# Kernel tuning notes

Hardware: AMD Instinct MI355X
Metric: run time of the kernel (lower is better)

## Reference

```python
import jax, jax.numpy as jnp
from jax import lax
import numpy as np

D_MODEL = 1024
D_STATE = 16
D_CONV = 4
EXPAND = 2
D_INNER = EXPAND * D_MODEL          # 2048
DT_RANK = D_MODEL // 16             # 64 (mamba 'auto' dt_rank)
B, L = 1, 1024


def setup_inputs() -> dict:
    key = jax.random.key(0)
    ks = jax.random.split(key, 8)

    def nrm(k, shape, s=0.02):
        return jax.random.normal(k, shape, jnp.float32) * s

    def mamba_params(kbase):
        k = jax.random.split(kbase, 7)
        return {
            'in_w': nrm(k[0], (2 * D_INNER, D_MODEL)),            # in_proj (no bias)
            'conv_w': nrm(k[1], (D_INNER, 1, D_CONV), 0.1),       # depthwise causal conv
            'conv_b': nrm(k[2], (D_INNER,), 0.1),
            'xproj_w': nrm(k[3], (DT_RANK + 2 * D_STATE, D_INNER)),
            'dt_w': nrm(k[4], (D_INNER, DT_RANK), 0.1),
            'dt_b': nrm(k[5], (D_INNER,), 0.1),
            'Alog': jnp.log(jnp.broadcast_to(jnp.arange(1., D_STATE + 1, dtype=jnp.float32), (D_INNER, D_STATE))),
            'Dp': jnp.ones((D_INNER,), jnp.float32),
            'out_w': nrm(k[6], (D_MODEL, D_INNER)),
        }

    fw = mamba_params(ks[0])
    bw = mamba_params(ks[1])
    inp = {'x': jax.random.normal(ks[2], (B, L, D_MODEL), jnp.float32)}
    for n, p in fw.items():
        inp['fw_' + n] = p
    for n, p in bw.items():
        inp['bw_' + n] = p
    inp['proj_w'] = nrm(ks[3], (D_MODEL, 2 * D_MODEL))
    inp['proj_b'] = jnp.zeros((D_MODEL,), jnp.float32)
    inp['ln_w'] = jnp.ones((D_MODEL,), jnp.float32)
    inp['ln_b'] = jnp.zeros((D_MODEL,), jnp.float32)
    return inp


def _mamba(x, in_w, conv_w, conv_b, xproj_w, dt_w, dt_b, Alog, Dp, out_w):
    # x: [B, L, d_model]
    xz = x @ in_w.T                                    # [B, L, 2*d_inner]
    xi, z = jnp.split(xz, 2, axis=-1)
    # causal depthwise conv over time
    xc = lax.conv_general_dilated(jnp.swapaxes(xi, 1, 2), conv_w, (1,),
                                  [(D_CONV - 1, 0)], feature_group_count=D_INNER)
    u = jnp.swapaxes(jax.nn.silu(xc + conv_b[None, :, None]), 1, 2)   # [B, L, d_inner]
    x_dbl = u @ xproj_w.T                              # [B, L, dt_rank + 2*d_state]
    dt = x_dbl[..., :DT_RANK]
    Bm = x_dbl[..., DT_RANK:DT_RANK + D_STATE]
    Cm = x_dbl[..., DT_RANK + D_STATE:]
    delta = jax.nn.softplus(dt @ dt_w.T + dt_b)        # [B, L, d_inner]
    A = -jnp.exp(Alog)                                 # [d_inner, d_state]
    dA = jnp.exp(jnp.einsum('bld,dn->bldn', delta, A))
    dBu = jnp.einsum('bld,bln,bld->bldn', delta, Bm, u)

    def step(h, inputs):
        a, b, c = inputs                               # a,b: [B,D,N]; c: [B,N]
        h = a * h + b
        return h, jnp.einsum('bdn,bn->bd', h, c)

    h0 = jnp.zeros((x.shape[0], D_INNER, D_STATE), x.dtype)
    _, ys = lax.scan(step, h0, (jnp.moveaxis(dA, 1, 0), jnp.moveaxis(dBu, 1, 0), jnp.moveaxis(Cm, 1, 0)))
    y = jnp.moveaxis(ys, 0, 1) + u * Dp                # [B, L, d_inner]
    return (y * jax.nn.silu(z)) @ out_w.T              # [B, L, d_model]


def _block(x,
           fw_in_w, fw_conv_w, fw_conv_b, fw_xproj_w, fw_dt_w, fw_dt_b, fw_Alog, fw_Dp, fw_out_w,
           bw_in_w, bw_conv_w, bw_conv_b, bw_xproj_w, bw_dt_w, bw_dt_b, bw_Alog, bw_Dp, bw_out_w,
           proj_w, proj_b, ln_w, ln_b):
    out_fw = _mamba(x, fw_in_w, fw_conv_w, fw_conv_b, fw_xproj_w, fw_dt_w, fw_dt_b, fw_Alog, fw_Dp, fw_out_w) + x
    xb = jnp.flip(x, axis=1)
    out_bw = jnp.flip(_mamba(xb, bw_in_w, bw_conv_w, bw_conv_b, bw_xproj_w, bw_dt_w, bw_dt_b, bw_Alog, bw_Dp, bw_out_w) + xb, axis=1)
    out = jnp.concatenate([out_fw, out_bw], axis=-1) @ proj_w.T + proj_b
    mu = out.mean(-1, keepdims=True)
    var = out.var(-1, keepdims=True)
    return (out - mu) / jnp.sqrt(var + 1e-5) * ln_w + ln_b


def reference(x,
              fw_in_w, fw_conv_w, fw_conv_b, fw_xproj_w, fw_dt_w, fw_dt_b, fw_Alog, fw_Dp, fw_out_w,
              bw_in_w, bw_conv_w, bw_conv_b, bw_xproj_w, bw_dt_w, bw_dt_b, bw_Alog, bw_Dp, bw_out_w,
              proj_w, proj_b, ln_w, ln_b):
    return _block(x,
                  fw_in_w, fw_conv_w, fw_conv_b, fw_xproj_w, fw_dt_w, fw_dt_b, fw_Alog, fw_Dp, fw_out_w,
                  bw_in_w, bw_conv_w, bw_conv_b, bw_xproj_w, bw_dt_w, bw_dt_b, bw_Alog, bw_Dp, bw_out_w,
                  proj_w, proj_b, ln_w, ln_b)
```

## Files before the change

kernel.cpp:

```cpp
#include <hip/hip_runtime.h>

typedef __bf16 bf16;
typedef __bf16 bf16x8 __attribute__((ext_vector_type(8)));
typedef float  f32x4  __attribute__((ext_vector_type(4)));

#define L_SEQ 1024
#define DM    1024
#define DI    2048
#define DTR   64
#define DSTATE 16
#define XD    96
#define NC    64
#define CS    16

__device__ __forceinline__ float bf2f(bf16 v){ return (float)v; }
__device__ __forceinline__ bf16  f2bf(float v){ return (bf16)v; }

__device__ __forceinline__ void gl_lds16(const bf16* g, bf16* l) {
  __builtin_amdgcn_global_load_lds(
      (const __attribute__((address_space(1))) unsigned int*)g,
      (__attribute__((address_space(3))) unsigned int*)l, 16, 0, 0);
}

#define OFF_X      0L
#define OFF_INW    1048576L
#define OFF_XPROJ  9437184L
#define OFF_DTW    9830400L
#define OFF_OUTW   10092544L
#define OFF_PROJW  14286848L
#define CVT_TOTAL  16384000L

__global__ __launch_bounds__(256) void cvt_k(
    const float* __restrict__ x,
    const float* __restrict__ inw0, const float* __restrict__ inw1,
    const float* __restrict__ xp0,  const float* __restrict__ xp1,
    const float* __restrict__ dt0,  const float* __restrict__ dt1,
    const float* __restrict__ ow0,  const float* __restrict__ ow1,
    const float* __restrict__ pw,   bf16* __restrict__ wb)
{
  long i = ((long)blockIdx.x * 256 + threadIdx.x) * 8;
  if (i >= CVT_TOTAL) return;
  const float* src; long off;
  if      (i < OFF_INW)                 { src = x;    off = i - OFF_X; }
  else if (i < OFF_INW + 4194304L)      { src = inw0; off = i - OFF_INW; }
  else if (i < OFF_XPROJ)               { src = inw1; off = i - (OFF_INW + 4194304L); }
  else if (i < OFF_XPROJ + 196608L)     { src = xp0;  off = i - OFF_XPROJ; }
  else if (i < OFF_DTW)                 { src = xp1;  off = i - (OFF_XPROJ + 196608L); }
  else if (i < OFF_DTW + 131072L)       { src = dt0;  off = i - OFF_DTW; }
  else if (i < OFF_OUTW)                { src = dt1;  off = i - (OFF_DTW + 131072L); }
  else if (i < OFF_OUTW + 2097152L)     { src = ow0;  off = i - OFF_OUTW; }
  else if (i < OFF_PROJW)               { src = ow1;  off = i - (OFF_OUTW + 2097152L); }
  else                                  { src = pw;   off = i - OFF_PROJW; }
  f32x4 v0 = *(const f32x4*)(src + off);
  f32x4 v1 = *(const f32x4*)(src + off + 4);
  bf16x8 t;
  #pragma unroll
  for (int q = 0; q < 4; q++) { t[q] = (bf16)v0[q]; t[4+q] = (bf16)v1[q]; }
  *(bf16x8*)(wb + i) = t;
}

template<int BM, int BN>
__global__ __launch_bounds__(256) void gemm_bt(
    const bf16* __restrict__ A, const bf16* __restrict__ B0, const bf16* __restrict__ B1,
    void* __restrict__ Cv, void* __restrict__ Cv2, int splitN,
    int M, int N, int K, int lda, int ldb, int ldc,
    long aOffZ, long cOffZ,
    const float* __restrict__ bias0, const float* __restrict__ bias1,
    int flipA1, int writeBf16, int act,
    const float* __restrict__ xF, int fuseRes)
{
  constexpr int WM = BM / 2, WN = BN / 2;
  constexpr int MI = WM / 16, NJ = WN / 16;
  constexpr int ACALLS = BM / 32;
  constexpr int BCALLS = BN / 32;

  const int tid  = threadIdx.x;
  const int z    = blockIdx.z;
  const bf16*  Bp   = z ? B1 : B0;
  const float* bias = z ? bias1 : bias0;
  const int flip = z ? flipA1 : 0;
  const int bm = blockIdx.x * BM;
  const int bn = blockIdx.y * BN;

  __shared__ bf16 As[BM * 64];
  __shared__ bf16 Bs[BN * 64];

  f32x4 acc[MI][NJ];
  #pragma unroll
  for (int i=0;i<MI;i++)
    #pragma unroll
    for (int j=0;j<NJ;j++) { acc[i][j][0]=0.f; acc[i][j][1]=0.f; acc[i][j][2]=0.f; acc[i][j][3]=0.f; }

  const int wave = tid >> 6;
  const int lane = tid & 63;
  const int wm = (wave >> 1) * WM;
  const int wn = (wave & 1) * WN;
  const int fr  = lane & 15;
  const int frx = fr & 7;
  const int kqc = lane >> 4;

  const bf16* aSrc[ACALLS];
  int aOff[ACALLS];
  #pragma unroll
  for (int t = 0; t < ACALLS; t++) {
    int s = (wave * ACALLS + t) * 64 + lane;
    int r = s >> 3;
    int j = (s & 7) ^ (r & 7);
    int ar = bm + r;
    int agr = flip ? (M - 1 - ar) : ar;
    aSrc[t] = A + (long)z * aOffZ + (long)agr * lda + j * 8;
    aOff[t] = (wave * ACALLS + t) * 512;
  }
  const bf16* bSrc[BCALLS];
  int bOff[BCALLS];
  #pragma unroll
  for (int t = 0; t < BCALLS; t++) {
    int s = (wave * BCALLS + t) * 64 + lane;
    int r = s >> 3;
    int j = (s & 7) ^ (r & 7);
    int br = bn + r; if (br > N - 1) br = N - 1;
    bSrc[t] = Bp + (long)br * ldb + j * 8;
    bOff[t] = (wave * BCALLS + t) * 512;
  }

  for (int k0 = 0; k0 < K; k0 += 64) {
    #pragma unroll
    for (int t = 0; t < ACALLS; t++) gl_lds16(aSrc[t] + k0, &As[aOff[t]]);
    #pragma unroll
    for (int t = 0; t < BCALLS; t++) gl_lds16(bSrc[t] + k0, &Bs[bOff[t]]);
    __syncthreads();

    #pragma unroll
    for (int ks8 = 0; ks8 < 8; ks8 += 4) {
      bf16x8 af[MI], bfr[NJ];
      #pragma unroll
      for (int i=0;i<MI;i++) {
        int row = wm + i*16 + fr;
        af[i]  = *(const bf16x8*)&As[(row * 8 + ((ks8 + kqc) ^ frx)) * 8];
      }
      #pragma unroll
      for (int j=0;j<NJ;j++) {
        int row = wn + j*16 + fr;
        bfr[j] = *(const bf16x8*)&Bs[(row * 8 + ((ks8 + kqc) ^ frx)) * 8];
      }
      #pragma unroll
      for (int i=0;i<MI;i++)
        #pragma unroll
        for (int j=0;j<NJ;j++)
          acc[i][j] = __builtin_amdgcn_mfma_f32_16x16x32_bf16(af[i], bfr[j], acc[i][j], 0, 0, 0);
    }
    __syncthreads();
  }

  const int rr = (lane >> 4) * 4;
  const int cc = lane & 15;
  #pragma unroll
  for (int i=0;i<MI;i++) {
    #pragma unroll
    for (int j=0;j<NJ;j++) {
      int gn = bn + wn + j*16 + cc;
      if (gn >= N) continue;
      float bv = bias ? bias[gn] : 0.f;
      #pragma unroll
      for (int r=0;r<4;r++) {
        int gm = bm + wm + i*16 + rr + r;
        float v = acc[i][j][r] + bv;
        if (fuseRes) {
          long row = z ? (long)(M - 1 - gm) : (long)gm;
          float o = v + xF[row * DM + gn];
          ((bf16*)Cv)[row * (2 * DM) + (long)z * DM + gn] = f2bf(o);
        } else {
          if (act == 1) v = fmaxf(v, 0.f) + __logf(1.f + __expf(-fabsf(v)));
          int gn2 = gn;
          void* Cp = Cv;
          if (gn >= splitN) { gn2 = gn - splitN; Cp = Cv2; }
          long idx = (long)z * cOffZ + (long)gm * ldc + gn2;
          if (writeBf16) ((bf16*)Cp)[idx] = f2bf(v);
          else           ((float*)Cp)[idx] = v;
        }
      }
    }
  }
}

__global__ __launch_bounds__(256) void conv_silu_k(
    const bf16* __restrict__ xi, const float* __restrict__ cw0, const float* __restrict__ cw1,
    const float* __restrict__ cb0, const float* __restrict__ cb1, bf16* __restrict__ u)
{
  int gid = blockIdx.x * 256 + threadIdx.x;
  int dir = gid >> 18;
  int rem = gid & ((1 << 18) - 1);
  int l = rem >> 8;
  int d0 = (rem & 255) * 8;
  const float* w = dir ? cw1 : cw0;
  const float* b = dir ? cb1 : cb0;
  const bf16* xid = xi + (long)dir * L_SEQ * DI;
  float acc[8];
  #pragma unroll
  for (int q = 0; q < 8; q++) acc[q] = b[d0 + q];
  #pragma unroll
  for (int j = 0; j < 4; j++) {
    int ll = l - 3 + j;
    if (ll < 0) continue;
    bf16x8 xv = *(const bf16x8*)(xid + (long)ll * DI + d0);
    #pragma unroll
    for (int q = 0; q < 8; q++) acc[q] += w[(d0 + q) * 4 + j] * bf2f(xv[q]);
  }
  bf16x8 o;
  #pragma unroll
  for (int q = 0; q < 8; q++) {
    float s = acc[q] / (1.f + __expf(-acc[q]));
    o[q] = f2bf(s);
  }
  *(bf16x8*)(u + (long)dir * L_SEQ * DI + (long)l * DI + d0) = o;
}

__global__ __launch_bounds__(256) void scan_p1(
    const bf16* __restrict__ delta, const bf16* __restrict__ u, const bf16* __restrict__ xdbl,
    const float* __restrict__ Alog0, const float* __restrict__ Alog1,
    bf16* __restrict__ hout, float* __restrict__ sumd)
{
  const int tid = threadIdx.x;
  const int c   = blockIdx.y;
  const int dir = blockIdx.z;
  const int d   = blockIdx.x * 256 + tid;
  const float* Alog = dir ? Alog1 : Alog0;
  const bf16* dl = delta + (long)dir * L_SEQ * DI;
  const bf16* ud = u     + (long)dir * L_SEQ * DI;
  const bf16* xd = xdbl  + (long)dir * L_SEQ * XD;
  const int l0 = c * CS;

  __shared__ float lb[CS][16];
  {
    int ll = tid >> 4, n = tid & 15;
    lb[ll][n] = bf2f(xd[(long)(l0 + ll) * XD + DTR + n]);
  }

  float dl_r[CS], uu_r[CS];
  #pragma unroll
  for (int s = 0; s < CS; s++) {
    dl_r[s] = bf2f(dl[(long)(l0 + s) * DI + d]);
    uu_r[s] = bf2f(ud[(long)(l0 + s) * DI + d]);
  }
  __syncthreads();

  float An[16], h[16];
  #pragma unroll
  for (int n = 0; n < 16; n++) { An[n] = -__expf(Alog[d * 16 + n]); h[n] = 0.f; }
  float sd = 0.f;

  #pragma unroll
  for (int ll = 0; ll < CS; ll++) {
    float dlt = dl_r[ll];
    sd += dlt;
    float du = dlt * uu_r[ll];
    #pragma unroll
    for (int n = 0; n < 16; n++) {
      float a = __expf(dlt * An[n]);
      h[n] = h[n] * a + du * lb[ll][n];
    }
  }

  bf16* hp = hout + (((long)dir * NC + c) * DI + d) * 16;
  bf16x8 o0, o1;
  #pragma unroll
  for (int n = 0; n < 8; n++) { o0[n] = f2bf(h[n]); o1[n] = f2bf(h[8 + n]); }
  *(bf16x8*)hp = o0;
  *(bf16x8*)(hp + 8) = o1;
  sumd[((long)dir * NC + c) * DI + d] = sd;
}

__global__ __launch_bounds__(256) void scan_p2(
    const float* __restrict__ Alog0, const float* __restrict__ Alog1,
    bf16* hout, const float* __restrict__ sumd)
{
  int g = blockIdx.x * 256 + threadIdx.x;
  int dir = g >> 15;
  int rem = g & 32767;
  int d = rem >> 4;
  int n = rem & 15;
  const float* Alog = dir ? Alog1 : Alog0;
  float An = -__expf(Alog[d * 16 + n]);
  float hs = 0.f;
  #pragma unroll 4
  for (int c = 0; c < NC; c++) {
    long base = ((long)dir * NC + c) * DI + d;
    float tmp = bf2f(hout[base * 16 + n]);
    float P = __expf(An * sumd[base]);
    hout[base * 16 + n] = f2bf(hs);
    hs = P * hs + tmp;
  }
}

__global__ __launch_bounds__(256) void scan_p3(
    const bf16* delta, const bf16* zb, const bf16* u, const bf16* __restrict__ xdbl,
    const float* __restrict__ Alog0, const float* __restrict__ Alog1,
    const float* __restrict__ Dp0, const float* __restrict__ Dp1,
    const bf16* __restrict__ hout, bf16* g)
{
  const int tid = threadIdx.x;
  const int c   = blockIdx.y;
  const int dir = blockIdx.z;
  const int d   = blockIdx.x * 256 + tid;
  const float* Alog = dir ? Alog1 : Alog0;
  const float* Dp   = dir ? Dp1 : Dp0;
  const bf16* dl = delta + (long)dir * L_SEQ * DI;
  const bf16* zd = zb    + (long)dir * L_SEQ * DI;
  const bf16* ud = u     + (long)dir * L_SEQ * DI;
  const bf16* xd = xdbl  + (long)dir * L_SEQ * XD;
  bf16* gd = g + (long)dir * L_SEQ * DI;
  const int l0 = c * CS;

  __shared__ float lb[CS][16];
  __shared__ float lc[CS][16];
  {
    int i = tid * 2;
    int ll = i >> 5, j = i & 31;
    const bf16* p = xd + (long)(l0 + ll) * XD + DTR + j;
    float v0 = bf2f(p[0]), v1 = bf2f(p[1]);
    if (j < 16) { lb[ll][j] = v0; lb[ll][j + 1] = v1; }
    else        { lc[ll][j - 16] = v0; lc[ll][j - 15] = v1; }
  }

  float dl_r[CS], uu_r[CS], zv_r[CS];
  #pragma unroll
  for (int s = 0; s < CS; s++) {
    dl_r[s] = bf2f(dl[(long)(l0 + s) * DI + d]);
    zv_r[s] = bf2f(zd[(long)(l0 + s) * DI + d]);
    uu_r[s] = bf2f(ud[(long)(l0 + s) * DI + d]);
  }
  const bf16* hp = hout + (((long)dir * NC + c) * DI + d) * 16;
  bf16x8 h0 = *(const bf16x8*)hp;
  bf16x8 h1 = *(const bf16x8*)(hp + 8);
  __syncthreads();

  float An[16], h[16];
  #pragma unroll
  for (int n = 0; n < 16; n++) {
    An[n] = -__expf(Alog[d * 16 + n]);
    h[n] = bf2f(n < 8 ? h0[n & 7] : h1[n & 7]);
  }
  const float Dpv = Dp[d];

  #pragma unroll
  for (int ll = 0; ll < CS; ll++) {
    float dlt = dl_r[ll];
    float du = dlt * uu_r[ll];
    float y = 0.f;
    #pragma unroll
    for (int n = 0; n < 16; n++) {
      float a = __expf(dlt * An[n]);
      h[n] = h[n] * a + du * lb[ll][n];
      y += h[n] * lc[ll][n];
    }
    y += uu_r[ll] * Dpv;
    float zv = zv_r[ll];
    float sz = zv / (1.f + __expf(-zv));
    gd[(long)(l0 + ll) * DI + d] = f2bf(y * sz);
  }
}

__global__ __launch_bounds__(256) void ln_k(
    const float* __restrict__ fin, const float* __restrict__ pb,
    const float* __restrict__ lnw, const float* __restrict__ lnb, float* __restrict__ out)
{
  int row = blockIdx.x;
  int tid = threadIdx.x;
  float v[4]; float s1 = 0.f, s2 = 0.f;
  #pragma unroll
  for (int j = 0; j < 4; j++) {
    int c = tid + j * 256;
    v[j] = fin[(long)row * DM + c] + pb[c];
    s1 += v[j]; s2 += v[j] * v[j];
  }
  #pragma unroll
  for (int off = 32; off; off >>= 1) { s1 += __shfl_down(s1, off); s2 += __shfl_down(s2, off); }
  __shared__ float red[8];
  int wave = tid >> 6, lane = tid & 63;
  if (lane == 0) { red[wave] = s1; red[4 + wave] = s2; }
  __syncthreads();
  float t1 = red[0] + red[1] + red[2] + red[3];
  float t2 = red[4] + red[5] + red[6] + red[7];
  float mu = t1 / DM;
  float var = t2 / DM - mu * mu;
  float inv = rsqrtf(var + 1e-5f);
  #pragma unroll
  for (int j = 0; j < 4; j++) {
    int c = tid + j * 256;
    out[(long)row * DM + c] = (v[j] - mu) * inv * lnw[c] + lnb[c];
  }
}

extern "C" void kernel_launch(void* const* d_in, const int* in_sizes, int n_in,
                              void* d_out, int out_size, void* d_ws, size_t ws_size,
                              hipStream_t stream)
{
  const float* x         = (const float*)d_in[0];
  const float* fw_conv_w = (const float*)d_in[2];
  const float* fw_conv_b = (const float*)d_in[3];
  const float* fw_dt_b   = (const float*)d_in[6];
  const float* fw_Alog   = (const float*)d_in[7];
  const float* fw_Dp     = (const float*)d_in[8];
  const float* bw_conv_w = (const float*)d_in[11];
  const float* bw_conv_b = (const float*)d_in[12];
  const float* bw_dt_b   = (const float*)d_in[15];
  const float* bw_Alog   = (const float*)d_in[16];
  const float* bw_Dp     = (const float*)d_in[17];
  const float* proj_b    = (const float*)d_in[20];
  const float* ln_w      = (const float*)d_in[21];
  const float* ln_b      = (const float*)d_in[22];

  char* ws = (char*)d_ws;
  const size_t MB = 1024 * 1024;
  bf16*  xi    = (bf16*)(ws + 0);
  bf16*  zb    = (bf16*)(ws + 8 * MB);
  bf16*  u     = (bf16*)(ws + 16 * MB);
  bf16*  xdbl  = (bf16*)(ws + 24 * MB);
  float* sumd  = (float*)(ws + 25 * MB);
  bf16*  hout  = (bf16*)(ws + 26 * MB);
  bf16*  wb    = (bf16*)(ws + 34 * MB);
  bf16*  g     = u;
  bf16*  delta = xi;
  bf16*  fused = (bf16*)(ws + 0);
  float* fin   = (float*)(ws + 4 * MB);

  bf16* xb     = wb + OFF_X;
  bf16* inw    = wb + OFF_INW;
  bf16* xprojw = wb + OFF_XPROJ;
  bf16* dtw    = wb + OFF_DTW;
  bf16* outw   = wb + OFF_OUTW;
  bf16* projw  = wb + OFF_PROJW;

  dim3 blk(256);
  const int BIGN = 1 << 30;

  cvt_k<<<(CVT_TOTAL / 8 + 255) / 256, blk, 0, stream>>>(
      x, (const float*)d_in[1], (const float*)d_in[10],
      (const float*)d_in[4], (const float*)d_in[13],
      (const float*)d_in[5], (const float*)d_in[14],
      (const float*)d_in[9], (const float*)d_in[18],
      (const float*)d_in[19], wb);

  gemm_bt<64,64><<<dim3(16, 64, 2), blk, 0, stream>>>(
      xb, inw, inw + 4194304L, (void*)xi, (void*)zb, 2048,
      1024, 4096, 1024, 1024, 1024, 2048,
      0L, (long)1024 * 2048, nullptr, nullptr, 1, 1, 0, nullptr, 0);

  conv_silu_k<<<2048, blk, 0, stream>>>(xi, fw_conv_w, bw_conv_w, fw_conv_b, bw_conv_b, u);

  gemm_bt<32,64><<<dim3(32, 2, 2), blk, 0, stream>>>(
      u, xprojw, xprojw + 196608L, (void*)xdbl, nullptr, BIGN,
      1024, 96, 2048, 2048, 2048, 96,
      (long)1024 * 2048, (long)1024 * 96, nullptr, nullptr, 0, 1, 0, nullptr, 0);

  gemm_bt<32,64><<<dim3(32, 32, 2), blk, 0, stream>>>(
      xdbl, dtw, dtw + 131072L, (void*)delta, nullptr, BIGN,
      1024, 2048, 64, 96, 64, 2048,
      (long)1024 * 96, (long)1024 * 2048, fw_dt_b, bw_dt_b, 0, 1, 1, nullptr, 0);

  scan_p1<<<dim3(8, NC, 2), blk, 0, stream>>>(delta, u, xdbl, fw_Alog, bw_Alog, hout, sumd);
  scan_p2<<<dim3(256), blk, 0, stream>>>(fw_Alog, bw_Alog, hout, sumd);
  scan_p3<<<dim3(8, NC, 2), blk, 0, stream>>>(delta, zb, u, xdbl, fw_Alog, bw_Alog,
                                              fw_Dp, bw_Dp, hout, g);

  gemm_bt<32,64><<<dim3(32, 16, 2), blk, 0, stream>>>(
      g, outw, outw + 2097152L, (void*)fused, nullptr, BIGN,
      1024, 1024, 2048, 2048, 2048, 1024,
      (long)1024 * 2048, 0L, nullptr, nullptr, 0, 1, 0, x, 1);

  gemm_bt<32,64><<<dim3(32, 16, 1), blk, 0, stream>>>(
      fused, projw, projw, (void*)fin, nullptr, BIGN,
      1024, 1024, 2048, 2048, 2048, 1024,
      0L, 0L, nullptr, nullptr, 0, 0, 0, nullptr, 0);

  ln_k<<<1024, blk, 0, stream>>>(fin, proj_b, ln_w, ln_b, (float*)d_out);
}
```

Measured before the change: 327.5 us.

## Fuse dt projection and softplus into scan phase-one kernel

```diff
diff --git a/kernel.cpp b/kernel.cpp
--- a/kernel.cpp
+++ b/kernel.cpp
@@ -216,33 +216,70 @@
 }
 
 __global__ __launch_bounds__(256) void scan_p1(
-    const bf16* __restrict__ delta, const bf16* __restrict__ u, const bf16* __restrict__ xdbl,
+    const bf16* __restrict__ u, const bf16* __restrict__ xdbl,
+    const bf16* __restrict__ dtw0, const bf16* __restrict__ dtw1,
+    const float* __restrict__ dtb0, const float* __restrict__ dtb1,
     const float* __restrict__ Alog0, const float* __restrict__ Alog1,
-    bf16* __restrict__ hout, float* __restrict__ sumd)
+    bf16* __restrict__ delta, bf16* __restrict__ hout, float* __restrict__ sumd)
 {
   const int tid = threadIdx.x;
   const int c   = blockIdx.y;
   const int dir = blockIdx.z;
   const int d   = blockIdx.x * 256 + tid;
   const float* Alog = dir ? Alog1 : Alog0;
-  const bf16* dl = delta + (long)dir * L_SEQ * DI;
-  const bf16* ud = u     + (long)dir * L_SEQ * DI;
-  const bf16* xd = xdbl  + (long)dir * L_SEQ * XD;
+  const bf16*  dtw  = (dir ? dtw1 : dtw0) + (long)d * DTR;
+  const float* dtb  = dir ? dtb1 : dtb0;
+  const bf16* ud = u    + (long)dir * L_SEQ * DI;
+  const bf16* xd = xdbl + (long)dir * L_SEQ * XD;
+  bf16* dl = delta + (long)dir * L_SEQ * DI;
   const int l0 = c * CS;
 
+  __shared__ float ldt[CS][64];
   __shared__ float lb[CS][16];
   {
-    int ll = tid >> 4, n = tid & 15;
-    lb[ll][n] = bf2f(xd[(long)(l0 + ll) * XD + DTR + n]);
-  }
-
-  float dl_r[CS], uu_r[CS];
-  #pragma unroll
-  for (int s = 0; s < CS; s++) {
-    dl_r[s] = bf2f(dl[(long)(l0 + s) * DI + d]);
+    int i = tid * 4;
+    int ll = i >> 6, k = i & 63;
+    const bf16* p = xd + (long)(l0 + ll) * XD + k;
+    ldt[ll][k]     = bf2f(p[0]);
+    ldt[ll][k + 1] = bf2f(p[1]);
+    ldt[ll][k + 2] = bf2f(p[2]);
+    ldt[ll][k + 3] = bf2f(p[3]);
+    int ll2 = tid >> 4, n = tid & 15;
+    lb[ll2][n] = bf2f(xd[(long)(l0 + ll2) * XD + DTR + n]);
+  }
+
+  float uu_r[CS];
+  #pragma unroll
+  for (int s = 0; s < CS; s++)
     uu_r[s] = bf2f(ud[(long)(l0 + s) * DI + d]);
-  }
+  bf16x8 dw[8];
+  #pragma unroll
+  for (int j = 0; j < 8; j++) dw[j] = *(const bf16x8*)(dtw + j * 8);
+  const float dtbv = dtb[d];
   __syncthreads();
+
+  float dl_r[CS];
+  #pragma unroll
+  for (int ll = 0; ll < CS; ll++) dl_r[ll] = dtbv;
+  #pragma unroll
+  for (int j = 0; j < 8; j++) {
+    float w0 = bf2f(dw[j][0]), w1 = bf2f(dw[j][1]), w2 = bf2f(dw[j][2]), w3 = bf2f(dw[j][3]);
+    float w4 = bf2f(dw[j][4]), w5 = bf2f(dw[j][5]), w6 = bf2f(dw[j][6]), w7 = bf2f(dw[j][7]);
+    #pragma unroll
+    for (int ll = 0; ll < CS; ll++) {
+      f32x4 a0 = *(const f32x4*)&ldt[ll][j * 8];
+      f32x4 a1 = *(const f32x4*)&ldt[ll][j * 8 + 4];
+      dl_r[ll] += w0*a0[0] + w1*a0[1] + w2*a0[2] + w3*a0[3]
+                + w4*a1[0] + w5*a1[1] + w6*a1[2] + w7*a1[3];
+    }
+  }
+  #pragma unroll
+  for (int ll = 0; ll < CS; ll++) {
+    float v = dl_r[ll];
+    float s = fmaxf(v, 0.f) + __logf(1.f + __expf(-fabsf(v)));
+    dl_r[ll] = s;
+    dl[(long)(l0 + ll) * DI + d] = f2bf(s);
+  }
 
   float An[16], h[16];
   #pragma unroll
@@ -453,12 +490,9 @@
       1024, 96, 2048, 2048, 2048, 96,
       (long)1024 * 2048, (long)1024 * 96, nullptr, nullptr, 0, 1, 0, nullptr, 0);
 
-  gemm_bt<32,64><<<dim3(32, 32, 2), blk, 0, stream>>>(
-      xdbl, dtw, dtw + 131072L, (void*)delta, nullptr, BIGN,
-      1024, 2048, 64, 96, 64, 2048,
-      (long)1024 * 96, (long)1024 * 2048, fw_dt_b, bw_dt_b, 0, 1, 1, nullptr, 0);
-
-  scan_p1<<<dim3(8, NC, 2), blk, 0, stream>>>(delta, u, xdbl, fw_Alog, bw_Alog, hout, sumd);
+  scan_p1<<<dim3(8, NC, 2), blk, 0, stream>>>(
+      u, xdbl, dtw, dtw + 131072L, fw_dt_b, bw_dt_b,
+      fw_Alog, bw_Alog, delta, hout, sumd);
   scan_p2<<<dim3(256), blk, 0, stream>>>(fw_Alog, bw_Alog, hout, sumd);
   scan_p3<<<dim3(8, NC, 2), blk, 0, stream>>>(delta, zb, u, xdbl, fw_Alog, bw_Alog,
                                               fw_Dp, bw_Dp, hout, g);
```

New measurement: 339.3 us. +3.6%, slower.
